# Performance work log

Hardware: AMD Instinct MI355X
Metric: run time of the kernel (lower is better)

Reference implementation:

```python
import jax, jax.numpy as jnp
import numpy as np

Q, S, D = 8192, 30, 512
THRESH = 30


def setup_inputs() -> dict:
    key = jax.random.key(0)
    ks = jax.random.split(key, 8)
    return {
        "query_encode": jax.random.normal(ks[0], (Q, D), jnp.float32),
        "support_encode": jax.random.normal(ks[1], (S, D), jnp.float32),
        # binary CTR-style labels in {0,1}
        "support_y": jnp.round(jax.random.uniform(ks[2], (1, S), jnp.float32)),
        "support_predict": jax.random.normal(ks[3], (S,), jnp.float32),
        "query_predict": jax.random.normal(ks[4], (Q,), jnp.float32),
        "fc1_w": jax.random.normal(ks[5], (D,), jnp.float32) / np.sqrt(D),
        "fc1_b": jnp.zeros((), jnp.float32),
        # AdjustLayer params: scale init 6, bias init 0, shape [THRESH, 1]
        "adjust_scale": jnp.full((THRESH, 1), 6.0, jnp.float32),
        "adjust_bias": jnp.zeros((THRESH, 1), jnp.float32),
        "num_samples": S,
    }


def reference(query_encode, support_encode, support_y, support_predict,
              query_predict, fc1_w, fc1_b, adjust_scale, adjust_bias,
              num_samples):
    # Pairwise L1 distance: [Q, S, D]
    distance = jnp.abs(query_encode[:, None, :] - support_encode[None, :, :])
    # Linear scorer over feature dim -> [Q, S]
    similar_score = jnp.einsum("qsd,d->qs", distance, fc1_w) + fc1_b
    attn = jax.nn.softmax(similar_score, axis=1)  # softmax over support dim
    # Residual of support labels vs predictor output: [1, S]
    delta_y = support_y - jax.nn.sigmoid(support_predict)[None, :]
    delta_y_hat = jnp.sum(delta_y * attn, axis=1)  # [Q]
    # AdjustLayer: indexed scale/bias (index is a static int here)
    scale = jnp.abs(adjust_scale[num_samples - 1, 0])
    bias = adjust_bias[num_samples - 1, 0]
    prediction = delta_y_hat * scale + bias + query_predict  # [Q]
    # Mean L2 distance to support set: [Q]
    mean_l2 = jnp.mean(jnp.sqrt(jnp.sum(distance ** 2, axis=-1)), axis=-1)
    return prediction, mean_l2
```

## Files before the change

### kernel.cpp

```cpp
#include <hip/hip_runtime.h>
#include <math.h>


#define QN 8192
#define SN 30
#define DN 512
#define BLK 512
#define WPB 8
#define QPW 4
#define QPB (WPB * QPW)
#define RS 515

__global__ __launch_bounds__(BLK, 2)
void resus_one(const float* __restrict__ query,
               const float* __restrict__ support,
               const float* __restrict__ support_y,
               const float* __restrict__ support_pr,
               const float* __restrict__ query_pr,
               const float* __restrict__ fc1_w,
               const float* __restrict__ adj_scale,
               const float* __restrict__ adj_bias,
               const int*   __restrict__ num_samples,
               float* __restrict__ out)
{
    __shared__ float s_lds[SN * RS];

    const int tid  = threadIdx.x;
    const int lane = tid & 63;
    const int wv   = tid >> 6;
    const int h    = lane >> 5;
    const int s    = lane & 31;
    const int srow_i = (s < SN) ? s : (SN - 1);

    const int qbase = blockIdx.x * QPB + wv * QPW;

    const float* qr0 = query + (size_t)(qbase + 0) * DN + h * 256;
    const float* qr1 = query + (size_t)(qbase + 1) * DN + h * 256;
    const float* qr2 = query + (size_t)(qbase + 2) * DN + h * 256;
    const float* qr3 = query + (size_t)(qbase + 3) * DN + h * 256;
    const float* wr  = fc1_w + h * 256;
    const float* srow = s_lds + srow_i * RS + h * 256;

    float4 c0a = *reinterpret_cast<const float4*>(qr0);
    float4 c0b = *reinterpret_cast<const float4*>(qr0 + 4);
    float4 c1a = *reinterpret_cast<const float4*>(qr1);
    float4 c1b = *reinterpret_cast<const float4*>(qr1 + 4);
    float4 c2a = *reinterpret_cast<const float4*>(qr2);
    float4 c2b = *reinterpret_cast<const float4*>(qr2 + 4);
    float4 c3a = *reinterpret_cast<const float4*>(qr3);
    float4 c3b = *reinterpret_cast<const float4*>(qr3 + 4);
    float4 cwa = *reinterpret_cast<const float4*>(wr);
    float4 cwb = *reinterpret_cast<const float4*>(wr + 4);

    {
        const float4* sg = reinterpret_cast<const float4*>(support);
        for (int i = tid; i < SN * (DN / 4); i += BLK) {
            const float4 v = sg[i];
            float* d = s_lds + (i >> 7) * RS + 4 * (i & 127);
            d[0] = v.x; d[1] = v.y; d[2] = v.z; d[3] = v.w;
        }
    }
    __syncthreads();

    float sc0 = 0.f, sq0 = 0.f, sc1 = 0.f, sq1 = 0.f;
    float sc2 = 0.f, sq2 = 0.f, sc3 = 0.f, sq3 = 0.f;

#define ACC8(CA, CB, SC, SQ) { float d_; \
    d_ = (CA).x - s0; SC = fmaf(cwa.x, fabsf(d_), SC); SQ = fmaf(d_, d_, SQ); \
    d_ = (CA).y - s1; SC = fmaf(cwa.y, fabsf(d_), SC); SQ = fmaf(d_, d_, SQ); \
    d_ = (CA).z - s2; SC = fmaf(cwa.z, fabsf(d_), SC); SQ = fmaf(d_, d_, SQ); \
    d_ = (CA).w - s3; SC = fmaf(cwa.w, fabsf(d_), SC); SQ = fmaf(d_, d_, SQ); \
    d_ = (CB).x - s4; SC = fmaf(cwb.x, fabsf(d_), SC); SQ = fmaf(d_, d_, SQ); \
    d_ = (CB).y - s5; SC = fmaf(cwb.y, fabsf(d_), SC); SQ = fmaf(d_, d_, SQ); \
    d_ = (CB).z - s6; SC = fmaf(cwb.z, fabsf(d_), SC); SQ = fmaf(d_, d_, SQ); \
    d_ = (CB).w - s7; SC = fmaf(cwb.w, fabsf(d_), SC); SQ = fmaf(d_, d_, SQ); }

#pragma unroll 4
    for (int j = 0; j < 32; ++j) {
        const int jn = (j + 1) & 31;
        float4 n0a = *reinterpret_cast<const float4*>(qr0 + 8 * jn);
        float4 n0b = *reinterpret_cast<const float4*>(qr0 + 8 * jn + 4);
        float4 n1a = *reinterpret_cast<const float4*>(qr1 + 8 * jn);
        float4 n1b = *reinterpret_cast<const float4*>(qr1 + 8 * jn + 4);
        float4 n2a = *reinterpret_cast<const float4*>(qr2 + 8 * jn);
        float4 n2b = *reinterpret_cast<const float4*>(qr2 + 8 * jn + 4);
        float4 n3a = *reinterpret_cast<const float4*>(qr3 + 8 * jn);
        float4 n3b = *reinterpret_cast<const float4*>(qr3 + 8 * jn + 4);
        float4 nwa = *reinterpret_cast<const float4*>(wr + 8 * jn);
        float4 nwb = *reinterpret_cast<const float4*>(wr + 8 * jn + 4);

        const float* sp = srow + 8 * j;
        const float s0 = sp[0], s1 = sp[1], s2 = sp[2], s3 = sp[3];
        const float s4 = sp[4], s5 = sp[5], s6 = sp[6], s7 = sp[7];

        ACC8(c0a, c0b, sc0, sq0)
        ACC8(c1a, c1b, sc1, sq1)
        ACC8(c2a, c2b, sc2, sq2)
        ACC8(c3a, c3b, sc3, sq3)

        c0a = n0a; c0b = n0b; c1a = n1a; c1b = n1b;
        c2a = n2a; c2b = n2b; c3a = n3a; c3b = n3b;
        cwa = nwa; cwb = nwb;
    }
#undef ACC8

    sc0 += __shfl_xor(sc0, 32); sq0 += __shfl_xor(sq0, 32);
    sc1 += __shfl_xor(sc1, 32); sq1 += __shfl_xor(sq1, 32);
    sc2 += __shfl_xor(sc2, 32); sq2 += __shfl_xor(sq2, 32);
    sc3 += __shfl_xor(sc3, 32); sq3 += __shfl_xor(sq3, 32);

    const bool valid = (s < SN);
    float dy = 0.f;
    if (valid)
        dy = support_y[s] - 1.0f / (1.0f + expf(-support_pr[s]));

    const int ns = num_samples[0];
    const float ascale = fabsf(adj_scale[ns - 1]);
    const float abias  = adj_bias[ns - 1];

    float scA = h ? sc2 : sc0;  float sqA = h ? sq2 : sq0;
    float scB = h ? sc3 : sc1;  float sqB = h ? sq3 : sq1;
    const int qA = qbase + 2 * h;
    const int qB = qA + 1;

#define FINISH(SCV, SQV, QI) { \
    float scv = (SCV), ssv = (SQV); \
    if (!valid) { scv = -1e30f; ssv = 0.f; } \
    float m_ = scv; \
    _Pragma("unroll") \
    for (int off = 16; off >= 1; off >>= 1) m_ = fmaxf(m_, __shfl_xor(m_, off)); \
    float e_   = valid ? expf(scv - m_) : 0.f; \
    float den_ = e_; \
    float num_ = dy * e_; \
    float l2_  = valid ? sqrtf(ssv) : 0.f; \
    _Pragma("unroll") \
    for (int off = 16; off >= 1; off >>= 1) { \
        den_ += __shfl_xor(den_, off); \
        num_ += __shfl_xor(num_, off); \
        l2_  += __shfl_xor(l2_,  off); \
    } \
    if (s == 0) { \
        out[(QI)]      = num_ / den_ * ascale + abias + query_pr[(QI)]; \
        out[QN + (QI)] = l2_ * (1.0f / (float)SN); \
    } }

    FINISH(scA, sqA, qA)
    FINISH(scB, sqB, qB)
#undef FINISH
}

extern "C" void kernel_launch(void* const* d_in, const int* in_sizes, int n_in,
                              void* d_out, int out_size, void* d_ws, size_t ws_size,
                              hipStream_t stream)
{
    const float* query      = (const float*)d_in[0];
    const float* support    = (const float*)d_in[1];
    const float* support_y  = (const float*)d_in[2];
    const float* support_pr = (const float*)d_in[3];
    const float* query_pr   = (const float*)d_in[4];
    const float* fc1_w      = (const float*)d_in[5];
    const float* adj_scale  = (const float*)d_in[7];
    const float* adj_bias   = (const float*)d_in[8];
    const int*   num_s      = (const int*)d_in[9];
    float* out = (float*)d_out;

    dim3 grid(QN / QPB);
    hipLaunchKernelGGL(resus_one, grid, dim3(BLK), 0, stream,
                       query, support, support_y, support_pr, query_pr,
                       fc1_w, adj_scale, adj_bias, num_s, out);
}
```

Before: 104.5 us.

## Split feature dim across wave pairs, reduce partials via LDS atomics, halve block queries

Each block now handles 16 queries instead of 32. Pairs of waves split the 512-wide feature dimension in half, so each thread runs 16 loop iterations instead of 32, and that loop is fully unrolled. Partial L1 scores and squared sums are combined through LDS atomics into a shared buffer, followed by a block barrier and one softmax finish per half-wave. The grid doubles in size, the launch bound allows more blocks per CU, and the LDS row padding changes. The aim is more parallelism and shorter per-thread serial chains, at the cost of extra atomics, a second barrier, and reloading the support rows into LDS for twice as many blocks.

```diff
diff --git a/kernel.cpp b/kernel.cpp
--- a/kernel.cpp
+++ b/kernel.cpp
@@ -6,12 +6,10 @@
 #define SN 30
 #define DN 512
 #define BLK 512
-#define WPB 8
-#define QPW 4
-#define QPB (WPB * QPW)
-#define RS 515
+#define QPB 16
+#define RS 513
 
-__global__ __launch_bounds__(BLK, 2)
+__global__ __launch_bounds__(BLK, 4)
 void resus_one(const float* __restrict__ query,
                const float* __restrict__ support,
                const float* __restrict__ support_y,
@@ -23,23 +21,26 @@
                const int*   __restrict__ num_samples,
                float* __restrict__ out)
 {
-    __shared__ float s_lds[SN * RS];
+    __shared__ float  s_lds[SN * RS];
+    __shared__ float2 part[QPB * SN];
 
     const int tid  = threadIdx.x;
     const int lane = tid & 63;
     const int wv   = tid >> 6;
+    const int p    = wv & 1;
     const int h    = lane >> 5;
     const int s    = lane & 31;
     const int srow_i = (s < SN) ? s : (SN - 1);
 
-    const int qbase = blockIdx.x * QPB + wv * QPW;
+    const int qbase = blockIdx.x * QPB + (wv >> 1) * 4;
+    const int doff  = p * 256 + h * 128;
 
-    const float* qr0 = query + (size_t)(qbase + 0) * DN + h * 256;
-    const float* qr1 = query + (size_t)(qbase + 1) * DN + h * 256;
-    const float* qr2 = query + (size_t)(qbase + 2) * DN + h * 256;
-    const float* qr3 = query + (size_t)(qbase + 3) * DN + h * 256;
-    const float* wr  = fc1_w + h * 256;
-    const float* srow = s_lds + srow_i * RS + h * 256;
+    const float* qr0 = query + (size_t)(qbase + 0) * DN + doff;
+    const float* qr1 = query + (size_t)(qbase + 1) * DN + doff;
+    const float* qr2 = query + (size_t)(qbase + 2) * DN + doff;
+    const float* qr3 = query + (size_t)(qbase + 3) * DN + doff;
+    const float* wr  = fc1_w + doff;
+    const float* srow = s_lds + srow_i * RS + doff;
 
     float4 c0a = *reinterpret_cast<const float4*>(qr0);
     float4 c0b = *reinterpret_cast<const float4*>(qr0 + 4);
@@ -59,6 +60,8 @@
             float* d = s_lds + (i >> 7) * RS + 4 * (i & 127);
             d[0] = v.x; d[1] = v.y; d[2] = v.z; d[3] = v.w;
         }
+        float* pf = reinterpret_cast<float*>(part);
+        for (int i = tid; i < QPB * SN * 2; i += BLK) pf[i] = 0.0f;
     }
     __syncthreads();
 
@@ -75,9 +78,9 @@
     d_ = (CB).z - s6; SC = fmaf(cwb.z, fabsf(d_), SC); SQ = fmaf(d_, d_, SQ); \
     d_ = (CB).w - s7; SC = fmaf(cwb.w, fabsf(d_), SC); SQ = fmaf(d_, d_, SQ); }
 
-#pragma unroll 4
-    for (int j = 0; j < 32; ++j) {
-        const int jn = (j + 1) & 31;
+#pragma unroll
+    for (int j = 0; j < 16; ++j) {
+        const int jn = (j + 1) & 15;
         float4 n0a = *reinterpret_cast<const float4*>(qr0 + 8 * jn);
         float4 n0b = *reinterpret_cast<const float4*>(qr0 + 8 * jn + 4);
         float4 n1a = *reinterpret_cast<const float4*>(qr1 + 8 * jn);
@@ -109,44 +112,53 @@
     sc2 += __shfl_xor(sc2, 32); sq2 += __shfl_xor(sq2, 32);
     sc3 += __shfl_xor(sc3, 32); sq3 += __shfl_xor(sq3, 32);
 
+    if (h == 0 && s < SN) {
+        const int qloc = (wv >> 1) * 4;
+        atomicAdd(&part[(qloc + 0) * SN + s].x, sc0);
+        atomicAdd(&part[(qloc + 0) * SN + s].y, sq0);
+        atomicAdd(&part[(qloc + 1) * SN + s].x, sc1);
+        atomicAdd(&part[(qloc + 1) * SN + s].y, sq1);
+        atomicAdd(&part[(qloc + 2) * SN + s].x, sc2);
+        atomicAdd(&part[(qloc + 2) * SN + s].y, sq2);
+        atomicAdd(&part[(qloc + 3) * SN + s].x, sc3);
+        atomicAdd(&part[(qloc + 3) * SN + s].y, sq3);
+    }
+    __syncthreads();
+
+    const int  qloc  = 2 * wv + h;
+    const int  q     = blockIdx.x * QPB + qloc;
     const bool valid = (s < SN);
-    float dy = 0.f;
+    const float2 pr  = part[qloc * SN + (valid ? s : 0)];
+
+    float scv = valid ? pr.x : -1e30f;
+    float ssv = valid ? pr.y : 0.f;
+    float dy  = 0.f;
     if (valid)
         dy = support_y[s] - 1.0f / (1.0f + expf(-support_pr[s]));
 
-    const int ns = num_samples[0];
-    const float ascale = fabsf(adj_scale[ns - 1]);
-    const float abias  = adj_bias[ns - 1];
+    float m = scv;
+#pragma unroll
+    for (int off = 16; off >= 1; off >>= 1)
+        m = fmaxf(m, __shfl_xor(m, off));
 
-    float scA = h ? sc2 : sc0;  float sqA = h ? sq2 : sq0;
-    float scB = h ? sc3 : sc1;  float sqB = h ? sq3 : sq1;
-    const int qA = qbase + 2 * h;
-    const int qB = qA + 1;
+    float e   = valid ? expf(scv - m) : 0.f;
+    float den = e;
+    float num = dy * e;
+    float l2  = valid ? sqrtf(ssv) : 0.f;
+#pragma unroll
+    for (int off = 16; off >= 1; off >>= 1) {
+        den += __shfl_xor(den, off);
+        num += __shfl_xor(num, off);
+        l2  += __shfl_xor(l2,  off);
+    }
 
-#define FINISH(SCV, SQV, QI) { \
-    float scv = (SCV), ssv = (SQV); \
-    if (!valid) { scv = -1e30f; ssv = 0.f; } \
-    float m_ = scv; \
-    _Pragma("unroll") \
-    for (int off = 16; off >= 1; off >>= 1) m_ = fmaxf(m_, __shfl_xor(m_, off)); \
-    float e_   = valid ? expf(scv - m_) : 0.f; \
-    float den_ = e_; \
-    float num_ = dy * e_; \
-    float l2_  = valid ? sqrtf(ssv) : 0.f; \
-    _Pragma("unroll") \
-    for (int off = 16; off >= 1; off >>= 1) { \
-        den_ += __shfl_xor(den_, off); \
-        num_ += __shfl_xor(num_, off); \
-        l2_  += __shfl_xor(l2_,  off); \
-    } \
-    if (s == 0) { \
-        out[(QI)]      = num_ / den_ * ascale + abias + query_pr[(QI)]; \
-        out[QN + (QI)] = l2_ * (1.0f / (float)SN); \
-    } }
-
-    FINISH(scA, sqA, qA)
-    FINISH(scB, sqB, qB)
-#undef FINISH
+    if (s == 0) {
+        const int ns = num_samples[0];
+        const float scale = fabsf(adj_scale[ns - 1]);
+        const float bias  = adj_bias[ns - 1];
+        out[q]      = num / den * scale + bias + query_pr[q];
+        out[QN + q] = l2 * (1.0f / (float)SN);
+    }
 }
 
 extern "C" void kernel_launch(void* const* d_in, const int* in_sizes, int n_in,
```

Result: no change. 106.5 us (+2.0%).
